# Performance work log

Measured on AMD Instinct MI355X. Metric: run time of the kernel, lower is better.

## Reference

```python
import jax, jax.numpy as jnp
import numpy as np
from jax import lax

KS = 3
N = KS * KS


def _conv(x, W, b, pad, stride):
    out = lax.conv_general_dilated(
        x, W, window_strides=(stride, stride),
        padding=[(pad, pad), (pad, pad)],
        dimension_numbers=("NCHW", "OIHW", "NCHW"))
    return out + b[None, :, None, None]


def setup_inputs() -> dict:
    key = jax.random.key(0)
    ks = jax.random.split(key, 5)
    b, c, h, w, outc = 16, 64, 64, 64, 128
    return {
        "x": jax.random.normal(ks[0], (b, c, h, w), jnp.float32),
        "W_off": jax.random.normal(ks[1], (2 * N, c, KS, KS), jnp.float32) * 0.05,
        "b_off": jax.random.normal(ks[2], (2 * N,), jnp.float32) * 0.05,
        "W_k": jax.random.normal(ks[3], (outc, c, KS, KS), jnp.float32) * 0.05,
        "b_k": jax.random.normal(ks[4], (outc,), jnp.float32) * 0.05,
    }


def _deform_conv(x, W_off, b_off, W_k, b_k):
    b, c, h, w = x.shape
    offset = _conv(x, W_off, b_off, pad=1, stride=1)  # [b, 2N, h, w]

    # kernel-grid offsets, flattened with x (row) index first: n = i*ks + j
    rng = jnp.arange(KS, dtype=x.dtype) - (KS - 1) // 2  # [-1, 0, 1]
    pnx = jnp.repeat(rng, KS)  # [N]
    pny = jnp.tile(rng, KS)    # [N]

    # sampling positions p = p0 + p_n + offset, clamped into the image
    px = jnp.arange(h, dtype=x.dtype)[None, None, :, None] + pnx[None, :, None, None] + offset[:, :N]
    py = jnp.arange(w, dtype=x.dtype)[None, None, None, :] + pny[None, :, None, None] + offset[:, N:]
    px = jnp.clip(px, 0, h - 1)
    py = jnp.clip(py, 0, w - 1)

    fx = jnp.floor(px)
    fy = jnp.floor(py)
    tx = px - fx  # fractional parts (bilinear weights)
    ty = py - fy
    x0 = fx.astype(jnp.int32)
    y0 = fy.astype(jnp.int32)
    x1 = jnp.minimum(x0 + 1, h - 1)  # out-of-range tap carries zero weight
    y1 = jnp.minimum(y0 + 1, w - 1)

    x_hw = x.transpose(0, 2, 3, 1).reshape(b, h * w, c)  # [b, hw, c]

    def gather(ix, iy):
        idx = (ix * w + iy).reshape(b, -1, 1)  # [b, N*h*w, 1]
        return jnp.take_along_axis(x_hw, idx, axis=1).reshape(b, N, h, w, c)

    wx0, wx1 = (1 - tx)[..., None], tx[..., None]
    wy0, wy1 = (1 - ty)[..., None], ty[..., None]
    # 4-tap bilinear interpolation == the original's sparse G @ x
    xo = (gather(x0, y0) * wx0 * wy0 + gather(x1, y0) * wx1 * wy0
          + gather(x0, y1) * wx0 * wy1 + gather(x1, y1) * wx1 * wy1)  # [b,N,h,w,c]

    # _reshape_x_offset: out[b,c, i_h*ks+i, i_w*ks+j] = xo[b, i*ks+j, i_h, i_w, c]
    xo = xo.reshape(b, KS, KS, h, w, c).transpose(0, 5, 3, 1, 4, 2)
    xo = xo.reshape(b, c, h * KS, w * KS)

    return _conv(xo, W_k, b_k, pad=0, stride=KS)  # [b, outc, h, w]


def reference(x, W_off, b_off, W_k, b_k):
    return _deform_conv(x, W_off, b_off, W_k, b_k)
```

## Files before the change

kernel.cpp:

```cpp
#include <hip/hip_runtime.h>

typedef __attribute__((ext_vector_type(8))) short bf16x8;
typedef __attribute__((ext_vector_type(4))) float floatx4;

__device__ __forceinline__ unsigned short f2bf(float f) {
    unsigned int u = __float_as_uint(f);
    u += 0x7FFFu + ((u >> 16) & 1u);
    return (unsigned short)(u >> 16);
}

__global__ __launch_bounds__(256) void prep_all(const float* __restrict__ x,
        const float* __restrict__ Wk, const float* __restrict__ Woff,
        unsigned short* __restrict__ xt, unsigned short* __restrict__ Wkb2,
        unsigned short* __restrict__ Woffb) {
    int bb = blockIdx.x;
    if (bb < 1024) {
        __shared__ float tile[64][65];
        int b = bb >> 6, y = bb & 63;
        const float* src = x + (size_t)b * 262144 + y * 64;
        int tx = threadIdx.x & 15, tg = threadIdx.x >> 4;
#pragma unroll
        for (int i = 0; i < 4; i++) {
            int c = tg + i * 16;
            float4 v = *(const float4*)(src + (size_t)c * 4096 + tx * 4);
            tile[c][tx * 4 + 0] = v.x; tile[c][tx * 4 + 1] = v.y;
            tile[c][tx * 4 + 2] = v.z; tile[c][tx * 4 + 3] = v.w;
        }
        __syncthreads();
        unsigned short* dst = xt + (size_t)bb * 4096;
#pragma unroll
        for (int i = 0; i < 4; i++) {
            int xc = tg + i * 16;
            int c4 = tx * 4;
            ushort4 v;
            v.x = f2bf(tile[c4 + 0][xc]); v.y = f2bf(tile[c4 + 1][xc]);
            v.z = f2bf(tile[c4 + 2][xc]); v.w = f2bf(tile[c4 + 3][xc]);
            *(ushort4*)(dst + xc * 64 + c4) = v;
        }
    } else if (bb < 1312) {
        int idx = (bb - 1024) * 256 + threadIdx.x;
        int tap = idx >> 13;
        int r = idx & 8191;
        int tile = r >> 9;
        int ln = (r >> 3) & 63;
        int j = r & 7;
        int mt = tile >> 1, kc = tile & 1;
        int oc = mt * 16 + (ln & 15);
        int c = kc * 32 + (ln >> 4) * 8 + j;
        Wkb2[idx] = f2bf(Wk[(oc * 64 + c) * 9 + tap]);
    } else {
        int idx = (bb - 1312) * 256 + threadIdx.x;
        int tap = idx >> 11;
        int r = idx & 2047;
        int tile = r >> 9;
        int ln = (r >> 3) & 63;
        int j = r & 7;
        int mt = tile >> 1, kc = tile & 1;
        int n = mt * 16 + (ln & 15);
        int c = kc * 32 + (ln >> 4) * 8 + j;
        float v = (n < 18) ? Woff[(n * 64 + c) * 9 + tap] : 0.f;
        Woffb[idx] = f2bf(v);
    }
}

__global__ __launch_bounds__(256, 4) void fused_kernel(
        const unsigned short* __restrict__ xt,
        const unsigned short* __restrict__ Wkb2,
        const unsigned short* __restrict__ Woffb,
        const float* __restrict__ boff,
        const float* __restrict__ bias,
        float* __restrict__ out) {
    __shared__ float offs[64][20];
    int tid = threadIdx.x;
    int wave = tid >> 6, lane = tid & 63;
    int frow = lane & 15, quad = lane >> 4;
    int bb = blockIdx.x;
    int xcd = bb & 7, idx = bb >> 3;
    int b = xcd * 2 + (idx >> 6);
    int pxBase = (idx & 63) * 64;
    int pl = wave * 16 + frow;
    int px = pxBase + pl;
    int y = px >> 6, xx = px & 63;
    const char* img = (const char*)(xt + (size_t)b * 262144) + quad * 16;
    const unsigned short* wofL = Woffb + lane * 8;
    const unsigned short* wkL  = Wkb2 + lane * 8;

    floatx4 acc1[2];
    acc1[0] = (floatx4)(0.f); acc1[1] = (floatx4)(0.f);
    for (int tap = 0; tap < 9; tap++) {
        int ry = y + tap / 3 - 1, rx = xx + tap % 3 - 1;
        bool valid = (ry >= 0) & (ry < 64) & (rx >= 0) & (rx < 64);
        const char* src = img + ((ry * 64 + rx) << 7);
        bf16x8 bz = {};
        const unsigned short* wt = wofL + tap * 2048;
#pragma unroll
        for (int kc = 0; kc < 2; kc++) {
            bf16x8 bfr = valid ? *(const bf16x8*)(src + kc * 64) : bz;
#pragma unroll
            for (int mt = 0; mt < 2; mt++) {
                bf16x8 af = *(const bf16x8*)(wt + (mt * 2 + kc) * 512);
                acc1[mt] = __builtin_amdgcn_mfma_f32_16x16x32_bf16(af, bfr, acc1[mt], 0, 0, 0);
            }
        }
    }
#pragma unroll
    for (int mt = 0; mt < 2; mt++)
#pragma unroll
        for (int rg = 0; rg < 4; rg++) {
            int n = mt * 16 + quad * 4 + rg;
            if (n < 18) offs[pl][n] = acc1[mt][rg] + boff[n];
        }
    __syncthreads();

    floatx4 acc[8];
#pragma unroll
    for (int i = 0; i < 8; i++) acc[i] = (floatx4)(0.f);

    for (int tap = 0; tap < 9; tap++) {
        float orow = offs[pl][tap];
        float ocol = offs[pl][9 + tap];
        float pr = (float)(y + tap / 3 - 1) + orow;
        float pc = (float)(xx + tap % 3 - 1) + ocol;
        pr = fminf(fmaxf(pr, 0.f), 63.f);
        pc = fminf(fmaxf(pc, 0.f), 63.f);
        float fr = floorf(pr), fc = floorf(pc);
        float tr = pr - fr, tc = pc - fc;
        int r0 = (int)fr, c0 = (int)fc;
        int r1 = min(r0 + 1, 63), c1 = min(c0 + 1, 63);
        float w00 = (1.f - tr) * (1.f - tc);
        float w01 = (1.f - tr) * tc;
        float w10 = tr * (1.f - tc);
        float w11 = tr * tc;
        int o00 = (r0 * 64 + c0) * 128;
        int o01 = (r0 * 64 + c1) * 128;
        int o10 = (r1 * 64 + c0) * 128;
        int o11 = (r1 * 64 + c1) * 128;
        const unsigned short* wt = wkL + tap * 8192;

#pragma unroll
        for (int kc = 0; kc < 2; kc++) {
            int4 u00 = __builtin_bit_cast(int4, *(const bf16x8*)(img + o00 + kc * 64));
            int4 u01 = __builtin_bit_cast(int4, *(const bf16x8*)(img + o01 + kc * 64));
            int4 u10 = __builtin_bit_cast(int4, *(const bf16x8*)(img + o10 + kc * 64));
            int4 u11 = __builtin_bit_cast(int4, *(const bf16x8*)(img + o11 + kc * 64));
            int4 r;
#pragma unroll
            for (int wd = 0; wd < 4; wd++) {
                int a00 = (wd == 0) ? u00.x : (wd == 1) ? u00.y : (wd == 2) ? u00.z : u00.w;
                int a01 = (wd == 0) ? u01.x : (wd == 1) ? u01.y : (wd == 2) ? u01.z : u01.w;
                int a10 = (wd == 0) ? u10.x : (wd == 1) ? u10.y : (wd == 2) ? u10.z : u10.w;
                int a11 = (wd == 0) ? u11.x : (wd == 1) ? u11.y : (wd == 2) ? u11.z : u11.w;
                float vl = w00 * __uint_as_float((unsigned)a00 << 16)
                         + w01 * __uint_as_float((unsigned)a01 << 16)
                         + w10 * __uint_as_float((unsigned)a10 << 16)
                         + w11 * __uint_as_float((unsigned)a11 << 16);
                float vh = w00 * __uint_as_float((unsigned)a00 & 0xffff0000u)
                         + w01 * __uint_as_float((unsigned)a01 & 0xffff0000u)
                         + w10 * __uint_as_float((unsigned)a10 & 0xffff0000u)
                         + w11 * __uint_as_float((unsigned)a11 & 0xffff0000u);
                unsigned pk = __builtin_amdgcn_perm(
                    __float_as_uint(vh) + 0x8000u,
                    __float_as_uint(vl) + 0x8000u, 0x07060302u);
                if (wd == 0) r.x = (int)pk; else if (wd == 1) r.y = (int)pk;
                else if (wd == 2) r.z = (int)pk; else r.w = (int)pk;
            }
            bf16x8 bfrag = __builtin_bit_cast(bf16x8, r);
#pragma unroll
            for (int mt = 0; mt < 8; mt++) {
                bf16x8 af = *(const bf16x8*)(wt + (mt * 2 + kc) * 512);
                acc[mt] = __builtin_amdgcn_mfma_f32_16x16x32_bf16(af, bfrag, acc[mt], 0, 0, 0);
            }
        }
    }

    float* outb = out + (size_t)b * 524288 + px;
#pragma unroll
    for (int mt = 0; mt < 8; mt++) {
#pragma unroll
        for (int rg = 0; rg < 4; rg++) {
            int oc = mt * 16 + quad * 4 + rg;
            outb[oc * 4096] = acc[mt][rg] + bias[oc];
        }
    }
}

extern "C" void kernel_launch(void* const* d_in, const int* in_sizes, int n_in,
                              void* d_out, int out_size, void* d_ws, size_t ws_size,
                              hipStream_t stream) {
    const float* x    = (const float*)d_in[0];
    const float* Woff = (const float*)d_in[1];
    const float* boff = (const float*)d_in[2];
    const float* Wk   = (const float*)d_in[3];
    const float* bk   = (const float*)d_in[4];
    float* out = (float*)d_out;

    char* ws = (char*)d_ws;
    unsigned short* xt    = (unsigned short*)ws;
    unsigned short* Wkb2  = (unsigned short*)(ws + 8388608);
    unsigned short* Woffb = (unsigned short*)(ws + 8536064);

    prep_all<<<1384, 256, 0, stream>>>(x, Wk, Woff, xt, Wkb2, Woffb);
    fused_kernel<<<1024, 256, 0, stream>>>(xt, Wkb2, Woffb, boff, bk, out);
}
```

Before: 144.4 us.

## Stage main-conv weights in double-buffered LDS and prefetch next tap's gathers

In the main deformable-conv loop, each tap's weight tile is now loaded cooperatively by all 256 threads into a double-buffered LDS array. Waves read their MFMA A fragments from LDS instead of each wave reloading them from global memory. The bilinear corner gathers and weights for the next tap are issued before the current tap's MFMAs, so gather latency overlaps compute. This adds 32 KB of LDS per block and a barrier per tap, which may lower occupancy under the 4-blocks launch bound and raise register pressure.

```diff
diff --git a/kernel.cpp b/kernel.cpp
--- a/kernel.cpp
+++ b/kernel.cpp
@@ -63,6 +63,32 @@
     }
 }
 
+__device__ __forceinline__ bf16x8 blend4(int4 u00, int4 u01, int4 u10, int4 u11,
+        float w00, float w01, float w10, float w11) {
+    int4 r;
+#pragma unroll
+    for (int wd = 0; wd < 4; wd++) {
+        int a00 = (wd == 0) ? u00.x : (wd == 1) ? u00.y : (wd == 2) ? u00.z : u00.w;
+        int a01 = (wd == 0) ? u01.x : (wd == 1) ? u01.y : (wd == 2) ? u01.z : u01.w;
+        int a10 = (wd == 0) ? u10.x : (wd == 1) ? u10.y : (wd == 2) ? u10.z : u10.w;
+        int a11 = (wd == 0) ? u11.x : (wd == 1) ? u11.y : (wd == 2) ? u11.z : u11.w;
+        float vl = w00 * __uint_as_float((unsigned)a00 << 16)
+                 + w01 * __uint_as_float((unsigned)a01 << 16)
+                 + w10 * __uint_as_float((unsigned)a10 << 16)
+                 + w11 * __uint_as_float((unsigned)a11 << 16);
+        float vh = w00 * __uint_as_float((unsigned)a00 & 0xffff0000u)
+                 + w01 * __uint_as_float((unsigned)a01 & 0xffff0000u)
+                 + w10 * __uint_as_float((unsigned)a10 & 0xffff0000u)
+                 + w11 * __uint_as_float((unsigned)a11 & 0xffff0000u);
+        unsigned pk = __builtin_amdgcn_perm(
+            __float_as_uint(vh) + 0x8000u,
+            __float_as_uint(vl) + 0x8000u, 0x07060302u);
+        if (wd == 0) r.x = (int)pk; else if (wd == 1) r.y = (int)pk;
+        else if (wd == 2) r.z = (int)pk; else r.w = (int)pk;
+    }
+    return __builtin_bit_cast(bf16x8, r);
+}
+
 __global__ __launch_bounds__(256, 4) void fused_kernel(
         const unsigned short* __restrict__ xt,
         const unsigned short* __restrict__ Wkb2,
@@ -70,6 +96,7 @@
         const float* __restrict__ boff,
         const float* __restrict__ bias,
         float* __restrict__ out) {
+    __shared__ unsigned short As[2][8192];
     __shared__ float offs[64][20];
     int tid = threadIdx.x;
     int wave = tid >> 6, lane = tid & 63;
@@ -83,10 +110,10 @@
     int y = px >> 6, xx = px & 63;
     const char* img = (const char*)(xt + (size_t)b * 262144) + quad * 16;
     const unsigned short* wofL = Woffb + lane * 8;
-    const unsigned short* wkL  = Wkb2 + lane * 8;
 
     floatx4 acc1[2];
     acc1[0] = (floatx4)(0.f); acc1[1] = (floatx4)(0.f);
+#pragma unroll
     for (int tap = 0; tap < 9; tap++) {
         int ry = y + tap / 3 - 1, rx = xx + tap % 3 - 1;
         bool valid = (ry >= 0) & (ry < 64) & (rx >= 0) & (rx < 64);
@@ -116,60 +143,89 @@
 #pragma unroll
     for (int i = 0; i < 8; i++) acc[i] = (floatx4)(0.f);
 
-    for (int tap = 0; tap < 9; tap++) {
-        float orow = offs[pl][tap];
-        float ocol = offs[pl][9 + tap];
-        float pr = (float)(y + tap / 3 - 1) + orow;
-        float pc = (float)(xx + tap % 3 - 1) + ocol;
+    bf16x8 aw[4];
+#pragma unroll
+    for (int i = 0; i < 4; i++)
+        aw[i] = *(const bf16x8*)(Wkb2 + i * 2048 + tid * 8);
+#pragma unroll
+    for (int i = 0; i < 4; i++)
+        *(bf16x8*)&As[0][i * 2048 + tid * 8] = aw[i];
+#pragma unroll
+    for (int i = 0; i < 4; i++)
+        aw[i] = *(const bf16x8*)(Wkb2 + 8192 + i * 2048 + tid * 8);
+
+    int4 c[8];
+    float w00, w01, w10, w11;
+    {
+        float orow = offs[pl][0], ocol = offs[pl][9];
+        float pr = (float)(y - 1) + orow;
+        float pc = (float)(xx - 1) + ocol;
         pr = fminf(fmaxf(pr, 0.f), 63.f);
         pc = fminf(fmaxf(pc, 0.f), 63.f);
         float fr = floorf(pr), fc = floorf(pc);
         float tr = pr - fr, tc = pc - fc;
         int r0 = (int)fr, c0 = (int)fc;
         int r1 = min(r0 + 1, 63), c1 = min(c0 + 1, 63);
-        float w00 = (1.f - tr) * (1.f - tc);
-        float w01 = (1.f - tr) * tc;
-        float w10 = tr * (1.f - tc);
-        float w11 = tr * tc;
-        int o00 = (r0 * 64 + c0) * 128;
-        int o01 = (r0 * 64 + c1) * 128;
-        int o10 = (r1 * 64 + c0) * 128;
-        int o11 = (r1 * 64 + c1) * 128;
-        const unsigned short* wt = wkL + tap * 8192;
-
+        w00 = (1.f - tr) * (1.f - tc); w01 = (1.f - tr) * tc;
+        w10 = tr * (1.f - tc);         w11 = tr * tc;
+        int o00 = (r0 * 64 + c0) * 128, o01 = (r0 * 64 + c1) * 128;
+        int o10 = (r1 * 64 + c0) * 128, o11 = (r1 * 64 + c1) * 128;
 #pragma unroll
         for (int kc = 0; kc < 2; kc++) {
-            int4 u00 = __builtin_bit_cast(int4, *(const bf16x8*)(img + o00 + kc * 64));
-            int4 u01 = __builtin_bit_cast(int4, *(const bf16x8*)(img + o01 + kc * 64));
-            int4 u10 = __builtin_bit_cast(int4, *(const bf16x8*)(img + o10 + kc * 64));
-            int4 u11 = __builtin_bit_cast(int4, *(const bf16x8*)(img + o11 + kc * 64));
-            int4 r;
-#pragma unroll
-            for (int wd = 0; wd < 4; wd++) {
-                int a00 = (wd == 0) ? u00.x : (wd == 1) ? u00.y : (wd == 2) ? u00.z : u00.w;
-                int a01 = (wd == 0) ? u01.x : (wd == 1) ? u01.y : (wd == 2) ? u01.z : u01.w;
-                int a10 = (wd == 0) ? u10.x : (wd == 1) ? u10.y : (wd == 2) ? u10.z : u10.w;
-                int a11 = (wd == 0) ? u11.x : (wd == 1) ? u11.y : (wd == 2) ? u11.z : u11.w;
-                float vl = w00 * __uint_as_float((unsigned)a00 << 16)
-                         + w01 * __uint_as_float((unsigned)a01 << 16)
-                         + w10 * __uint_as_float((unsigned)a10 << 16)
-                         + w11 * __uint_as_float((unsigned)a11 << 16);
-                float vh = w00 * __uint_as_float((unsigned)a00 & 0xffff0000u)
-                         + w01 * __uint_as_float((unsigned)a01 & 0xffff0000u)
-                         + w10 * __uint_as_float((unsigned)a10 & 0xffff0000u)
-                         + w11 * __uint_as_float((unsigned)a11 & 0xffff0000u);
-                unsigned pk = __builtin_amdgcn_perm(
-                    __float_as_uint(vh) + 0x8000u,
-                    __float_as_uint(vl) + 0x8000u, 0x07060302u);
-                if (wd == 0) r.x = (int)pk; else if (wd == 1) r.y = (int)pk;
-                else if (wd == 2) r.z = (int)pk; else r.w = (int)pk;
+            c[0 + kc] = *(const int4*)(img + o00 + kc * 64);
+            c[2 + kc] = *(const int4*)(img + o01 + kc * 64);
+            c[4 + kc] = *(const int4*)(img + o10 + kc * 64);
+            c[6 + kc] = *(const int4*)(img + o11 + kc * 64);
+        }
+    }
+
+#pragma unroll
+    for (int tap = 0; tap < 9; tap++) {
+        __syncthreads();
+        bf16x8 bfrag[2];
+#pragma unroll
+        for (int kc = 0; kc < 2; kc++)
+            bfrag[kc] = blend4(c[0 + kc], c[2 + kc], c[4 + kc], c[6 + kc],
+                               w00, w01, w10, w11);
+        if (tap < 8) {
+            int nt = tap + 1;
+            float orow = offs[pl][nt], ocol = offs[pl][9 + nt];
+            float pr = (float)(y + nt / 3 - 1) + orow;
+            float pc = (float)(xx + nt % 3 - 1) + ocol;
+            pr = fminf(fmaxf(pr, 0.f), 63.f);
+            pc = fminf(fmaxf(pc, 0.f), 63.f);
+            float fr = floorf(pr), fc = floorf(pc);
+            float tr = pr - fr, tc = pc - fc;
+            int r0 = (int)fr, c0 = (int)fc;
+            int r1 = min(r0 + 1, 63), c1 = min(c0 + 1, 63);
+            w00 = (1.f - tr) * (1.f - tc); w01 = (1.f - tr) * tc;
+            w10 = tr * (1.f - tc);         w11 = tr * tc;
+            int o00 = (r0 * 64 + c0) * 128, o01 = (r0 * 64 + c1) * 128;
+            int o10 = (r1 * 64 + c0) * 128, o11 = (r1 * 64 + c1) * 128;
+#pragma unroll
+            for (int kc = 0; kc < 2; kc++) {
+                c[0 + kc] = *(const int4*)(img + o00 + kc * 64);
+                c[2 + kc] = *(const int4*)(img + o01 + kc * 64);
+                c[4 + kc] = *(const int4*)(img + o10 + kc * 64);
+                c[6 + kc] = *(const int4*)(img + o11 + kc * 64);
             }
-            bf16x8 bfrag = __builtin_bit_cast(bf16x8, r);
+        }
+        const unsigned short* abuf = &As[tap & 1][0];
+#pragma unroll
+        for (int kc = 0; kc < 2; kc++)
 #pragma unroll
             for (int mt = 0; mt < 8; mt++) {
-                bf16x8 af = *(const bf16x8*)(wt + (mt * 2 + kc) * 512);
-                acc[mt] = __builtin_amdgcn_mfma_f32_16x16x32_bf16(af, bfrag, acc[mt], 0, 0, 0);
+                bf16x8 af = *(const bf16x8*)&abuf[(mt * 2 + kc) * 512 + lane * 8];
+                acc[mt] = __builtin_amdgcn_mfma_f32_16x16x32_bf16(af, bfrag[kc], acc[mt], 0, 0, 0);
             }
+        if (tap < 8) {
+#pragma unroll
+            for (int i = 0; i < 4; i++)
+                *(bf16x8*)&As[(tap + 1) & 1][i * 2048 + tid * 8] = aw[i];
+            if (tap < 7)
+#pragma unroll
+                for (int i = 0; i < 4; i++)
+                    aw[i] = *(const bf16x8*)(Wkb2 + (tap + 2) * 8192 + i * 2048 + tid * 8);
         }
     }
 
```

Result: faster. 133.2 us (-7.7%).
